# Performance work log

Measured on AMD Instinct MI355X. Metric: run time of the kernel, lower is better.

The kernel has to match this reference:

```python
import jax, jax.numpy as jnp
import numpy as np

B, L, H, C, A = 8, 4096, 512, 64, 512
NEG = -1000000000.0

def setup_inputs() -> dict:
    key = jax.random.key(0)
    ks = jax.random.split(key, 6)
    hidden_states = jax.random.normal(ks[0], (B, L, H), dtype=jnp.float32)
    critical_mask = jax.random.randint(ks[1], (B, L, 1), 0, 2).astype(bool)
    count_active_channels = jax.random.randint(ks[2], (B, L, 1), 0, 64).astype(jnp.int32)
    channel_activity = jax.random.normal(ks[3], (B, L, C), dtype=jnp.float32)
    proj_w = jax.random.normal(ks[4], (H, A), dtype=jnp.float32) * 0.02
    proj_b = jnp.zeros((A,), dtype=jnp.float32)
    score_w = jax.random.normal(ks[5], (A, 1), dtype=jnp.float32) * 0.02
    score_b = jnp.zeros((1,), dtype=jnp.float32)
    return {"hidden_states": hidden_states, "critical_mask": critical_mask,
            "count_active_channels": count_active_channels,
            "channel_activity": channel_activity,
            "proj_w": proj_w, "proj_b": proj_b,
            "score_w": score_w, "score_b": score_b}

def reference(hidden_states, critical_mask, count_active_channels, channel_activity,
              proj_w, proj_b, score_w, score_b):
    mask = critical_mask[..., 0].astype(bool)                       # (B,L)
    count_signal = count_active_channels[..., 0].astype(hidden_states.dtype)  # (B,L)
    activity = jnp.maximum(channel_activity.astype(hidden_states.dtype), 0.0)  # (B,L,C)
    # score(tanh(proj(h)))  -> (B,L)
    logits = (jnp.tanh(hidden_states @ proj_w + proj_b) @ score_w + score_b)[..., 0]
    logits = logits + jnp.log1p(jnp.maximum(count_signal, 0.0))
    channel_mask = activity > 0                                      # (B,L,C)
    # (B,C,L) masked logits with log1p activity bias
    channel_logits = logits[:, None, :] + jnp.log1p(jnp.swapaxes(activity, 1, 2))
    channel_logits = jnp.where(jnp.swapaxes(channel_mask, 1, 2), channel_logits, NEG)
    has_channel_any = channel_mask.any(axis=1)                       # (B,C)
    weights = jax.nn.softmax(channel_logits, axis=-1)                # (B,C,L)
    weights = jnp.where(has_channel_any[..., None], weights, 0.0)
    channel_contexts = jnp.einsum('bcl,blh->bch', weights, hidden_states)  # (B,C,H)
    fallback = jnp.broadcast_to(hidden_states[:, -1:, :], channel_contexts.shape)
    channel_contexts = jnp.where(has_channel_any[..., None], channel_contexts, fallback)
    mix = activity / jnp.maximum(activity.sum(axis=2, keepdims=True), 1.0)  # (B,L,C)
    expanded_context = jnp.einsum('blc,bch->blh', mix, channel_contexts)    # (B,L,H)
    max_count = jnp.maximum(count_signal.max(axis=1, keepdims=True), 1.0)
    density_gate = 1.0 + count_signal / max_count                    # (B,L)
    attended = jnp.where(mask[..., None], expanded_context * density_gate[..., None], hidden_states)
    return attended, weights
```

## Files before the change

kernel.cpp:

```cpp
#include <hip/hip_runtime.h>
#include <hip/hip_bf16.h>
#include <math.h>

#define NEGV (-1000000000.0f)
constexpr int Bb = 8, Ll = 4096, Hh = 512, Cc = 64, Aa = 512;

typedef float f32x4 __attribute__((ext_vector_type(4)));
typedef short s16x8 __attribute__((ext_vector_type(8)));

__device__ inline ushort f2bf(float f) {
  union { float f; uint u; } v; v.f = f;
  uint u = v.u;
  return (ushort)((u + 0x7FFFu + ((u >> 16) & 1u)) >> 16);
}

__device__ inline uint bfpack2(float x, float y) {
  __hip_bfloat162 h = __float22bfloat162_rn(make_float2(x, y));
  union { __hip_bfloat162 h; uint u; } v; v.h = h;
  return v.u;
}

__device__ __forceinline__ void gl16(const void* g, void* l) {
  __builtin_amdgcn_global_load_lds(
      reinterpret_cast<const __attribute__((address_space(1))) unsigned int*>(
          reinterpret_cast<uintptr_t>(g)),
      reinterpret_cast<__attribute__((address_space(3))) unsigned int*>(
          reinterpret_cast<uintptr_t>(l)),
      16, 0, 0);
}

__global__ void k_cvtT(const float* __restrict__ hid, ushort* __restrict__ hidb,
                       ushort* __restrict__ hidbT) {
  __shared__ ushort s[64][65];
  const int b = blockIdx.z;
  const int l0 = blockIdx.x * 64;
  const int h0 = blockIdx.y * 64;
  const int tid = threadIdx.x;
  const int lr = tid >> 6;
  const int hc = tid & 63;
#pragma unroll
  for (int i = 0; i < 16; ++i) {
    int l = lr + i * 4;
    ushort v = f2bf(hid[((size_t)(b * Ll + l0 + l)) * Hh + h0 + hc]);
    s[l][hc] = v;
    hidb[((size_t)(b * Ll + l0 + l)) * Hh + h0 + hc] = v;
  }
  __syncthreads();
#pragma unroll
  for (int i = 0; i < 8; ++i) {
    int e = tid + i * 256;
    int ht = e >> 5, p = e & 31;
    uint v = (uint)s[2 * p][ht] | ((uint)s[2 * p + 1][ht] << 16);
    *(uint*)(hidbT + ((size_t)(b * Hh + h0 + ht)) * Ll + l0 + 2 * p) = v;
  }
}

__global__ void k_init(const int* __restrict__ cnt, const float* __restrict__ sb,
                       float* __restrict__ logits, int* __restrict__ cmax) {
  int i = blockIdx.x * 256 + threadIdx.x;
  int c = cnt[i];
  logits[i] = sb[0] + log1pf(fmaxf((float)c, 0.f));
  int m = c;
#pragma unroll
  for (int s = 32; s; s >>= 1) m = max(m, __shfl_xor(m, s));
  if ((threadIdx.x & 63) == 0) atomicMax(&cmax[i >> 12], m);
}

__global__ void kT_pw(const float* __restrict__ pw, ushort* __restrict__ pwT) {
  __shared__ ushort s[64][65];
  const int k0 = (blockIdx.x >> 3) * 64, a0 = (blockIdx.x & 7) * 64;
  const int t = threadIdx.x;
#pragma unroll
  for (int i = 0; i < 16; ++i) {
    int e = t + i * 256;
    int kk = e >> 6, aa = e & 63;
    s[aa][kk] = f2bf(pw[(size_t)(k0 + kk) * Aa + a0 + aa]);
  }
  __syncthreads();
#pragma unroll
  for (int i = 0; i < 16; ++i) {
    int e = t + i * 256;
    int aa = e >> 6, kk = e & 63;
    pwT[(size_t)(a0 + aa) * Hh + k0 + kk] = s[aa][kk];
  }
}

__global__ __launch_bounds__(256) void k0_gemm(
    const ushort* __restrict__ hidb, const ushort* __restrict__ pwT,
    const float* __restrict__ pb, const float* __restrict__ sw,
    float* __restrict__ logits) {
  __shared__ ushort smem[16384];
  const int bm = blockIdx.x, bn = blockIdx.y;
  const int tid = threadIdx.x;
  const int lane = tid & 63;
  const int w = tid >> 6;
  const int wm = w >> 1, wn = w & 1;
  const int lc = lane & 15, lq = lane >> 4;

  const int srow = tid >> 2;
  const int schunk = (tid & 3) * 8;
  const ushort* Ag = hidb + ((size_t)(bm * 128 + srow)) * Hh + schunk;
  const ushort* Bg = pwT + ((size_t)(bn * 128 + srow)) * Hh + schunk;
  const int wrow = 16 * w;

  f32x4 acc[4][4];
#pragma unroll
  for (int mi = 0; mi < 4; ++mi)
#pragma unroll
    for (int ni = 0; ni < 4; ++ni) acc[mi][ni] = (f32x4){0.f, 0.f, 0.f, 0.f};

  const int aoffc = (wm * 64 + lc) * 32 + lq * 8;
  const int boffc = (wn * 64 + lc) * 32 + lq * 8;

#define K0_STAGE(buf, kb)                                   \
  do {                                                      \
    const ushort* ag = Ag + (kb) * 32;                      \
    const ushort* bg = Bg + (kb) * 32;                      \
    ushort* la = smem + (buf) * 4096 + wrow * 32;           \
    ushort* lb = smem + 8192 + (buf) * 4096 + wrow * 32;    \
    gl16(ag, la);                                           \
    gl16(ag + 64 * Hh, la + 64 * 32);                       \
    gl16(bg, lb);                                           \
    gl16(bg + 64 * Hh, lb + 64 * 32);                       \
  } while (0)

  K0_STAGE(0, 0);
  __syncthreads();

  int buf = 0;
  for (int kb = 0; kb < 16; ++kb) {
    if (kb < 15) K0_STAGE(buf ^ 1, kb + 1);
    const ushort* Ab = smem + buf * 4096;
    const ushort* Bt = smem + 8192 + buf * 4096;
    s16x8 af[4], bfr[4];
#pragma unroll
    for (int mi = 0; mi < 4; ++mi)
      af[mi] = *(const s16x8*)(Ab + aoffc + mi * 512);
#pragma unroll
    for (int ni = 0; ni < 4; ++ni)
      bfr[ni] = *(const s16x8*)(Bt + boffc + ni * 512);
#pragma unroll
    for (int mi = 0; mi < 4; ++mi)
#pragma unroll
      for (int ni = 0; ni < 4; ++ni)
        acc[mi][ni] = __builtin_amdgcn_mfma_f32_16x16x32_bf16(
            af[mi], bfr[ni], acc[mi][ni], 0, 0, 0);
    __syncthreads();
    buf ^= 1;
  }
#undef K0_STAGE

  float pbv[4], swv[4];
#pragma unroll
  for (int ni = 0; ni < 4; ++ni) {
    int n = bn * 128 + wn * 64 + ni * 16 + lc;
    pbv[ni] = pb[n];
    swv[ni] = sw[n];
  }
#pragma unroll
  for (int mi = 0; mi < 4; ++mi) {
#pragma unroll
    for (int r = 0; r < 4; ++r) {
      float s = 0.f;
#pragma unroll
      for (int ni = 0; ni < 4; ++ni) {
        float x = acc[mi][ni][r] + pbv[ni];
        float e = __expf(2.f * x);
        float th = 1.f - 2.f / (e + 1.f);
        s = fmaf(th, swv[ni], s);
      }
      s += __shfl_xor(s, 1);
      s += __shfl_xor(s, 2);
      s += __shfl_xor(s, 4);
      s += __shfl_xor(s, 8);
      if (lc == 0) {
        int m = bm * 128 + wm * 64 + mi * 16 + lq * 4 + r;
        atomicAdd(&logits[m], s);
      }
    }
  }
}

__global__ void k2_transpose(const float* __restrict__ act,
                             float* __restrict__ actT,
                             float* __restrict__ dinv) {
  __shared__ float t64[64][65];
  const int b = blockIdx.x >> 6;
  const int l0 = (blockIdx.x & 63) * 64;
  const int tid = threadIdx.x;
#pragma unroll
  for (int i = 0; i < 16; ++i) {
    int e = tid + i * 256;
    int l = e >> 6, c = e & 63;
    float v = act[((size_t)(b * Ll + l0 + l)) * Cc + c];
    t64[l][c] = fmaxf(v, 0.f);
  }
  __syncthreads();
  if (tid < 64) {
    float s = 0.f;
#pragma unroll 8
    for (int c = 0; c < 64; ++c) s += t64[tid][c];
    dinv[b * Ll + l0 + tid] = 1.0f / fmaxf(s, 1.0f);
  }
#pragma unroll
  for (int i = 0; i < 16; ++i) {
    int e = tid + i * 256;
    int c = e >> 6, lq = e & 63;
    actT[((size_t)(b * Cc + c)) * Ll + l0 + lq] = t64[lq][c];
  }
}

__global__ void k3_softmax(const float* __restrict__ actT,
                           const float* __restrict__ logits,
                           float* __restrict__ wout,
                           ushort* __restrict__ wb16,
                           int* __restrict__ hasany) {
  __shared__ float rmax[4], rcnt[4], rsum[4];
  const int bid = blockIdx.x;
  const int b = bid >> 6;
  const int tid = threadIdx.x;
  const float* arow = actT + (size_t)bid * Ll;

  float xs[16];
  float lmax = NEGV, fcnt = 0.f;
#pragma unroll
  for (int i = 0; i < 16; ++i) {
    int l = tid + i * 256;
    float a = arow[l];
    float x;
    if (a > 0.f) {
      x = logits[b * Ll + l] + log1pf(a);
      fcnt += 1.f;
    } else {
      x = NEGV;
    }
    xs[i] = x;
    lmax = fmaxf(lmax, x);
  }
#pragma unroll
  for (int m = 32; m >= 1; m >>= 1) {
    lmax = fmaxf(lmax, __shfl_xor(lmax, m));
    fcnt += __shfl_xor(fcnt, m);
  }
  if ((tid & 63) == 0) { rmax[tid >> 6] = lmax; rcnt[tid >> 6] = fcnt; }
  __syncthreads();
  float m4 = fmaxf(fmaxf(rmax[0], rmax[1]), fmaxf(rmax[2], rmax[3]));
  float call = rcnt[0] + rcnt[1] + rcnt[2] + rcnt[3];

  float lsum = 0.f;
#pragma unroll
  for (int i = 0; i < 16; ++i) {
    float e = expf(xs[i] - m4);
    xs[i] = e;
    lsum += e;
  }
#pragma unroll
  for (int m = 32; m >= 1; m >>= 1) lsum += __shfl_xor(lsum, m);
  if ((tid & 63) == 0) rsum[tid >> 6] = lsum;
  __syncthreads();
  float s = rsum[0] + rsum[1] + rsum[2] + rsum[3];
  int any = call > 0.5f;
  float inv = any ? 1.0f / s : 0.f;
#pragma unroll
  for (int i = 0; i < 16; ++i) {
    float wv = xs[i] * inv;
    wout[(size_t)bid * Ll + tid + i * 256] = wv;
    wb16[(size_t)bid * Ll + tid + i * 256] = f2bf(wv);
  }
  if (tid == 0) hasany[bid] = any;
}

__global__ __launch_bounds__(256) void k5_mfma(
    const ushort* __restrict__ wb16, const ushort* __restrict__ hidbT,
    float* __restrict__ pbuf) {
  const int b = blockIdx.x, nt = blockIdx.y, kz = blockIdx.z;
  const int tid = threadIdx.x;
  const int w = tid >> 6, lane = tid & 63;
  const int lc = lane & 15, lq = lane >> 4;
  const int h0 = nt * 128 + w * 32;

  f32x4 acc[4][2];
#pragma unroll
  for (int mi = 0; mi < 4; ++mi)
#pragma unroll
    for (int ni = 0; ni < 2; ++ni) acc[mi][ni] = (f32x4){0.f, 0.f, 0.f, 0.f};

  const ushort* Abase =
      wb16 + (size_t)b * Cc * Ll + (size_t)lc * Ll + kz * 256 + lq * 8;
  const ushort* Bbase =
      hidbT + ((size_t)(b * Hh + h0 + lc)) * Ll + kz * 256 + lq * 8;

#pragma unroll 2
  for (int kb = 0; kb < 8; ++kb) {
    s16x8 af[4];
#pragma unroll
    for (int mi = 0; mi < 4; ++mi)
      af[mi] = *(const s16x8*)(Abase + (size_t)mi * 16 * Ll + kb * 32);
    s16x8 bfv[2];
#pragma unroll
    for (int ni = 0; ni < 2; ++ni)
      bfv[ni] = *(const s16x8*)(Bbase + (size_t)ni * 16 * Ll + kb * 32);
#pragma unroll
    for (int mi = 0; mi < 4; ++mi)
#pragma unroll
      for (int ni = 0; ni < 2; ++ni)
        acc[mi][ni] = __builtin_amdgcn_mfma_f32_16x16x32_bf16(
            af[mi], bfv[ni], acc[mi][ni], 0, 0, 0);
  }

  const size_t obase = ((size_t)(kz * Bb + b)) * Cc * Hh;
#pragma unroll
  for (int mi = 0; mi < 4; ++mi)
#pragma unroll
    for (int ni = 0; ni < 2; ++ni)
#pragma unroll
      for (int r = 0; r < 4; ++r)
        pbuf[obase + (size_t)(mi * 16 + lq * 4 + r) * Hh + h0 + ni * 16 + lc] =
            acc[mi][ni][r];
}

__global__ void k6_reduce(const float* __restrict__ pbuf,
                          const int* __restrict__ hasany,
                          const float* __restrict__ hid,
                          float* __restrict__ cctx) {
  int idx = blockIdx.x * 256 + threadIdx.x;
  float s = 0.f;
#pragma unroll
  for (int z = 0; z < 16; ++z) s += pbuf[(size_t)z * 262144 + idx];
  int bc = idx >> 9, b = idx >> 15, h = idx & 511;
  cctx[idx] = hasany[bc] ? s : hid[((size_t)(b * Ll + Ll - 1)) * Hh + h];
}

__global__ __launch_bounds__(256) void k7_out(
    const float* __restrict__ hid, const float* __restrict__ act,
    const float* __restrict__ dinv, const float* __restrict__ cctx,
    const int* __restrict__ mask, const int* __restrict__ cnt,
    const int* __restrict__ cmax, float* __restrict__ out) {
  __shared__ float cct[64][128];
  __shared__ float mixs[64][64];
  __shared__ float gateb[64];
  __shared__ int maskb[64];
  const int b = blockIdx.x;
  const int l0 = blockIdx.y * 64;
  const int h0 = blockIdx.z * 128;
  const int tid = threadIdx.x;
  const int w = tid >> 6;

  {
    const float* g = cctx + (size_t)(b * Cc + (tid >> 5)) * Hh + h0 + (tid & 31) * 4;
    float* lb = &cct[0][0] + (2 * w) * 128;
#pragma unroll
    for (int i = 0; i < 8; ++i)
      gl16(g + (size_t)(i * 8) * Hh, lb + i * 8 * 128);
  }
#pragma unroll
  for (int i = 0; i < 4; ++i) {
    int e = tid + i * 256;
    int t = e >> 4, c4 = (e & 15) * 4;
    float4 a4 = *(const float4*)(act + ((size_t)(b * Ll + l0 + t)) * Cc + c4);
    float dv = dinv[b * Ll + l0 + t];
    a4.x = fmaxf(a4.x, 0.f) * dv;
    a4.y = fmaxf(a4.y, 0.f) * dv;
    a4.z = fmaxf(a4.z, 0.f) * dv;
    a4.w = fmaxf(a4.w, 0.f) * dv;
    *(float4*)&mixs[t][c4] = a4;
  }
  if (tid < 64) {
    int l = l0 + tid;
    maskb[tid] = mask[b * Ll + l];
    gateb[tid] = 1.0f + (float)cnt[b * Ll + l] / fmaxf((float)cmax[b], 1.0f);
  }
  __syncthreads();

  const int hcol = (tid & 31) * 4;
  const int tok0 = (tid >> 5) * 8;

  f32x4 acc[8];
#pragma unroll
  for (int t = 0; t < 8; ++t) acc[t] = (f32x4){0.f, 0.f, 0.f, 0.f};

#pragma unroll 4
  for (int c0 = 0; c0 < 64; c0 += 4) {
    f32x4 cv0 = *(const f32x4*)&cct[c0 + 0][hcol];
    f32x4 cv1 = *(const f32x4*)&cct[c0 + 1][hcol];
    f32x4 cv2 = *(const f32x4*)&cct[c0 + 2][hcol];
    f32x4 cv3 = *(const f32x4*)&cct[c0 + 3][hcol];
#pragma unroll
    for (int t = 0; t < 8; ++t) {
      f32x4 mv = *(const f32x4*)&mixs[tok0 + t][c0];
      f32x4 a = acc[t];
      a = cv0 * mv.x + a;
      a = cv1 * mv.y + a;
      a = cv2 * mv.z + a;
      a = cv3 * mv.w + a;
      acc[t] = a;
    }
  }

#pragma unroll
  for (int t = 0; t < 8; ++t) {
    int tok = tok0 + t;
    size_t off = ((size_t)(b * Ll + l0 + tok)) * Hh + h0 + hcol;
    f32x4 o;
    if (maskb[tok]) {
      o = acc[t] * gateb[tok];
    } else {
      o = *(const f32x4*)(hid + off);
    }
    *(f32x4*)(out + off) = o;
  }
}

extern "C" void kernel_launch(void* const* d_in, const int* in_sizes, int n_in,
                              void* d_out, int out_size, void* d_ws,
                              size_t ws_size, hipStream_t stream) {
  const float* hid = (const float*)d_in[0];
  const int* mask = (const int*)d_in[1];
  const int* cnt = (const int*)d_in[2];
  const float* act = (const float*)d_in[3];
  const float* pw = (const float*)d_in[4];
  const float* pb = (const float*)d_in[5];
  const float* sw = (const float*)d_in[6];
  const float* sb = (const float*)d_in[7];

  float* out_att = (float*)d_out;
  float* out_w = out_att + (size_t)Bb * Ll * Hh;

  float* ws = (float*)d_ws;
  float* cctx = ws;
  int* cmaxi = (int*)(ws + 262144);
  float* logits = ws + 262152;
  float* actT = ws + 294920;
  float* dinv = ws + 2392072;
  int* hasany = (int*)(ws + 2424840);
  ushort* pwT = (ushort*)(ws + 2425352);
  ushort* wb16 = (ushort*)(ws + 2556424);
  float* pbuf = ws + 3605000;

  ushort* hidb = (ushort*)out_att;
  ushort* hidbT = (ushort*)(out_att + 8388608);

  hipMemsetAsync(cmaxi, 0, 8 * sizeof(int), stream);

  k_cvtT<<<dim3(64, 8, 8), 256, 0, stream>>>(hid, hidb, hidbT);
  k_init<<<128, 256, 0, stream>>>(cnt, sb, logits, cmaxi);
  kT_pw<<<64, 256, 0, stream>>>(pw, pwT);
  k0_gemm<<<dim3(256, 4), 256, 0, stream>>>(hidb, pwT, pb, sw, logits);
  k2_transpose<<<512, 256, 0, stream>>>(act, actT, dinv);
  k3_softmax<<<512, 256, 0, stream>>>(actT, logits, out_w, wb16, hasany);
  k5_mfma<<<dim3(8, 4, 16), 256, 0, stream>>>(wb16, hidbT, pbuf);
  k6_reduce<<<1024, 256, 0, stream>>>(pbuf, hasany, hid, cctx);
  k7_out<<<dim3(8, 64, 4), 256, 0, stream>>>(hid, act, dinv, cctx, mask, cnt,
                                             cmaxi, out_att);
}
```

Measured before the change: 265.0 us.

## Replace activity transpose and row softmax with online split-L softmax stats

```diff
diff --git a/kernel.cpp b/kernel.cpp
--- a/kernel.cpp
+++ b/kernel.cpp
@@ -12,12 +12,6 @@
   union { float f; uint u; } v; v.f = f;
   uint u = v.u;
   return (ushort)((u + 0x7FFFu + ((u >> 16) & 1u)) >> 16);
-}
-
-__device__ inline uint bfpack2(float x, float y) {
-  __hip_bfloat162 h = __float22bfloat162_rn(make_float2(x, y));
-  union { __hip_bfloat162 h; uint u; } v; v.h = h;
-  return v.u;
 }
 
 __device__ __forceinline__ void gl16(const void* g, void* l) {
@@ -31,28 +25,35 @@
 
 __global__ void k_cvtT(const float* __restrict__ hid, ushort* __restrict__ hidb,
                        ushort* __restrict__ hidbT) {
-  __shared__ ushort s[64][65];
+  __shared__ ushort s[64][66];
   const int b = blockIdx.z;
   const int l0 = blockIdx.x * 64;
   const int h0 = blockIdx.y * 64;
   const int tid = threadIdx.x;
-  const int lr = tid >> 6;
-  const int hc = tid & 63;
-#pragma unroll
-  for (int i = 0; i < 16; ++i) {
-    int l = lr + i * 4;
-    ushort v = f2bf(hid[((size_t)(b * Ll + l0 + l)) * Hh + h0 + hc]);
-    s[l][hc] = v;
-    hidb[((size_t)(b * Ll + l0 + l)) * Hh + h0 + hc] = v;
-  }
-  __syncthreads();
+  const int lr = tid >> 5;
+  const int hc2 = (tid & 31) * 2;
 #pragma unroll
   for (int i = 0; i < 8; ++i) {
-    int e = tid + i * 256;
-    int ht = e >> 5, p = e & 31;
-    uint v = (uint)s[2 * p][ht] | ((uint)s[2 * p + 1][ht] << 16);
-    *(uint*)(hidbT + ((size_t)(b * Hh + h0 + ht)) * Ll + l0 + 2 * p) = v;
-  }
+    int l = lr * 8 + i;
+    float2 f = *(const float2*)(hid + ((size_t)(b * Ll + l0 + l)) * Hh + h0 + hc2);
+    ushort v0 = f2bf(f.x), v1 = f2bf(f.y);
+    *(uint*)(hidb + ((size_t)(b * Ll + l0 + l)) * Hh + h0 + hc2) =
+        (uint)v0 | ((uint)v1 << 16);
+    s[l][hc2] = v0;
+    s[l][hc2 + 1] = v1;
+  }
+  __syncthreads();
+  const int ht = tid >> 2;
+  const int d0 = (tid & 3) * 8;
+  uint v[8];
+#pragma unroll
+  for (int k = 0; k < 8; ++k) {
+    int p = d0 + k;
+    v[k] = (uint)s[2 * p][ht] | ((uint)s[2 * p + 1][ht] << 16);
+  }
+  ushort* dst = hidbT + ((size_t)(b * Hh + h0 + ht)) * Ll + l0 + 2 * d0;
+  *(uint4*)dst = (uint4){v[0], v[1], v[2], v[3]};
+  *(uint4*)(dst + 8) = (uint4){v[4], v[5], v[6], v[7]};
 }
 
 __global__ void k_init(const int* __restrict__ cnt, const float* __restrict__ sb,
@@ -181,93 +182,128 @@
   }
 }
 
-__global__ void k2_transpose(const float* __restrict__ act,
-                             float* __restrict__ actT,
-                             float* __restrict__ dinv) {
-  __shared__ float t64[64][65];
-  const int b = blockIdx.x >> 6;
-  const int l0 = (blockIdx.x & 63) * 64;
-  const int tid = threadIdx.x;
-#pragma unroll
-  for (int i = 0; i < 16; ++i) {
-    int e = tid + i * 256;
-    int l = e >> 6, c = e & 63;
-    float v = act[((size_t)(b * Ll + l0 + l)) * Cc + c];
-    t64[l][c] = fmaxf(v, 0.f);
+__global__ __launch_bounds__(256) void k2_stats(
+    const float* __restrict__ act, const float* __restrict__ logits,
+    float* __restrict__ dinv, float* __restrict__ part) {
+  __shared__ float Ms[16][64], Ss[16][64];
+  const int b = blockIdx.x, lt = blockIdx.y;
+  const int tid = threadIdx.x;
+  const int r = tid >> 4, cg = (tid & 15) * 4;
+
+  float m[4] = {NEGV, NEGV, NEGV, NEGV};
+  float s[4] = {0.f, 0.f, 0.f, 0.f};
+
+#pragma unroll
+  for (int i = 0; i < 8; ++i) {
+    int l = lt * 128 + r + 16 * i;
+    float lg = logits[b * Ll + l];
+    float4 a4 = *(const float4*)(act + ((size_t)(b * Ll + l)) * Cc + cg);
+    float av[4] = {a4.x, a4.y, a4.z, a4.w};
+    float rsum = 0.f;
+#pragma unroll
+    for (int j = 0; j < 4; ++j) {
+      float a = fmaxf(av[j], 0.f);
+      rsum += a;
+      if (a > 0.f) {
+        float x = lg + log1pf(a);
+        float mn = fmaxf(m[j], x);
+        s[j] = s[j] * expf(m[j] - mn) + expf(x - mn);
+        m[j] = mn;
+      }
+    }
+    rsum += __shfl_xor(rsum, 1);
+    rsum += __shfl_xor(rsum, 2);
+    rsum += __shfl_xor(rsum, 4);
+    rsum += __shfl_xor(rsum, 8);
+    if ((tid & 15) == 0) dinv[b * Ll + l] = 1.0f / fmaxf(rsum, 1.0f);
+  }
+
+#pragma unroll
+  for (int j = 0; j < 4; ++j) {
+    Ms[r][cg + j] = m[j];
+    Ss[r][cg + j] = s[j];
   }
   __syncthreads();
   if (tid < 64) {
-    float s = 0.f;
+    float gm = NEGV, gs = 0.f;
+#pragma unroll
+    for (int rr = 0; rr < 16; ++rr) {
+      float mm = Ms[rr][tid], ss = Ss[rr][tid];
+      float mn = fmaxf(gm, mm);
+      gs = gs * expf(gm - mn) + ss * expf(mm - mn);
+      gm = mn;
+    }
+    size_t o = (((size_t)(b * Cc + tid)) * 32 + lt) * 2;
+    part[o] = gm;
+    part[o + 1] = gs;
+  }
+}
+
+__global__ void k2_merge(const float* __restrict__ part, float* __restrict__ gm,
+                         float* __restrict__ ginv, int* __restrict__ hasany) {
+  int g = blockIdx.x * 256 + threadIdx.x;
+  const float* p = part + (size_t)g * 64;
+  float m = NEGV, s = 0.f;
 #pragma unroll 8
-    for (int c = 0; c < 64; ++c) s += t64[tid][c];
-    dinv[b * Ll + l0 + tid] = 1.0f / fmaxf(s, 1.0f);
-  }
-#pragma unroll
-  for (int i = 0; i < 16; ++i) {
-    int e = tid + i * 256;
-    int c = e >> 6, lq = e & 63;
-    actT[((size_t)(b * Cc + c)) * Ll + l0 + lq] = t64[lq][c];
-  }
-}
-
-__global__ void k3_softmax(const float* __restrict__ actT,
-                           const float* __restrict__ logits,
-                           float* __restrict__ wout,
-                           ushort* __restrict__ wb16,
-                           int* __restrict__ hasany) {
-  __shared__ float rmax[4], rcnt[4], rsum[4];
-  const int bid = blockIdx.x;
-  const int b = bid >> 6;
-  const int tid = threadIdx.x;
-  const float* arow = actT + (size_t)bid * Ll;
-
-  float xs[16];
-  float lmax = NEGV, fcnt = 0.f;
-#pragma unroll
-  for (int i = 0; i < 16; ++i) {
-    int l = tid + i * 256;
-    float a = arow[l];
-    float x;
-    if (a > 0.f) {
-      x = logits[b * Ll + l] + log1pf(a);
-      fcnt += 1.f;
-    } else {
-      x = NEGV;
-    }
-    xs[i] = x;
-    lmax = fmaxf(lmax, x);
-  }
-#pragma unroll
-  for (int m = 32; m >= 1; m >>= 1) {
-    lmax = fmaxf(lmax, __shfl_xor(lmax, m));
-    fcnt += __shfl_xor(fcnt, m);
-  }
-  if ((tid & 63) == 0) { rmax[tid >> 6] = lmax; rcnt[tid >> 6] = fcnt; }
-  __syncthreads();
-  float m4 = fmaxf(fmaxf(rmax[0], rmax[1]), fmaxf(rmax[2], rmax[3]));
-  float call = rcnt[0] + rcnt[1] + rcnt[2] + rcnt[3];
-
-  float lsum = 0.f;
-#pragma unroll
-  for (int i = 0; i < 16; ++i) {
-    float e = expf(xs[i] - m4);
-    xs[i] = e;
-    lsum += e;
-  }
-#pragma unroll
-  for (int m = 32; m >= 1; m >>= 1) lsum += __shfl_xor(lsum, m);
-  if ((tid & 63) == 0) rsum[tid >> 6] = lsum;
-  __syncthreads();
-  float s = rsum[0] + rsum[1] + rsum[2] + rsum[3];
-  int any = call > 0.5f;
-  float inv = any ? 1.0f / s : 0.f;
-#pragma unroll
-  for (int i = 0; i < 16; ++i) {
-    float wv = xs[i] * inv;
-    wout[(size_t)bid * Ll + tid + i * 256] = wv;
-    wb16[(size_t)bid * Ll + tid + i * 256] = f2bf(wv);
-  }
-  if (tid == 0) hasany[bid] = any;
+  for (int t = 0; t < 32; ++t) {
+    float mm = p[2 * t], ss = p[2 * t + 1];
+    float mn = fmaxf(m, mm);
+    s = s * expf(m - mn) + ss * expf(mm - mn);
+    m = mn;
+  }
+  int any = s > 0.5f;
+  gm[g] = m;
+  ginv[g] = any ? 1.0f / s : 0.f;
+  hasany[g] = any;
+}
+
+__global__ __launch_bounds__(256) void k3_weights(
+    const float* __restrict__ act, const float* __restrict__ logits,
+    const float* __restrict__ gm, const float* __restrict__ ginv,
+    float* __restrict__ wout, ushort* __restrict__ wb16) {
+  __shared__ float wls[128][68];
+  const int b = blockIdx.x, lt = blockIdx.y;
+  const int tid = threadIdx.x;
+  const int r = tid >> 4, cg = (tid & 15) * 4;
+
+  float gm4[4], gi4[4];
+#pragma unroll
+  for (int j = 0; j < 4; ++j) {
+    gm4[j] = gm[b * Cc + cg + j];
+    gi4[j] = ginv[b * Cc + cg + j];
+  }
+
+#pragma unroll
+  for (int i = 0; i < 8; ++i) {
+    int l = lt * 128 + r + 16 * i;
+    float lg = logits[b * Ll + l];
+    float4 a4 = *(const float4*)(act + ((size_t)(b * Ll + l)) * Cc + cg);
+    float av[4] = {a4.x, a4.y, a4.z, a4.w};
+    f32x4 wv;
+#pragma unroll
+    for (int j = 0; j < 4; ++j) {
+      float a = fmaxf(av[j], 0.f);
+      float x = lg + log1pf(a);
+      wv[j] = (a > 0.f) ? expf(x - gm4[j]) * gi4[j] : 0.f;
+    }
+    *(f32x4*)&wls[r + 16 * i][cg] = wv;
+  }
+  __syncthreads();
+
+  const int c = tid >> 2;
+  const int ch = (tid & 3) * 32;
+  float* wo = wout + ((size_t)(b * Cc + c)) * Ll + lt * 128 + ch;
+  ushort* wbo = wb16 + ((size_t)(b * Cc + c)) * Ll + lt * 128 + ch;
+#pragma unroll
+  for (int q = 0; q < 8; ++q) {
+    float4 v = make_float4(wls[ch + 4 * q + 0][c], wls[ch + 4 * q + 1][c],
+                           wls[ch + 4 * q + 2][c], wls[ch + 4 * q + 3][c]);
+    *(float4*)(wo + 4 * q) = v;
+    uint2 u;
+    u.x = (uint)f2bf(v.x) | ((uint)f2bf(v.y) << 16);
+    u.y = (uint)f2bf(v.z) | ((uint)f2bf(v.w) << 16);
+    *(uint2*)(wbo + 4 * q) = u;
+  }
 }
 
 __global__ __launch_bounds__(256) void k5_mfma(
@@ -430,12 +466,14 @@
   float* cctx = ws;
   int* cmaxi = (int*)(ws + 262144);
   float* logits = ws + 262152;
-  float* actT = ws + 294920;
-  float* dinv = ws + 2392072;
-  int* hasany = (int*)(ws + 2424840);
-  ushort* pwT = (ushort*)(ws + 2425352);
-  ushort* wb16 = (ushort*)(ws + 2556424);
-  float* pbuf = ws + 3605000;
+  float* dinv = ws + 294920;
+  int* hasany = (int*)(ws + 327688);
+  float* gmbuf = ws + 328200;
+  float* ginvbuf = ws + 328712;
+  float* part = ws + 329224;
+  ushort* pwT = (ushort*)(ws + 361992);
+  ushort* wb16 = (ushort*)(ws + 493064);
+  float* pbuf = ws + 1541640;
 
   ushort* hidb = (ushort*)out_att;
   ushort* hidbT = (ushort*)(out_att + 8388608);
@@ -446,8 +484,10 @@
   k_init<<<128, 256, 0, stream>>>(cnt, sb, logits, cmaxi);
   kT_pw<<<64, 256, 0, stream>>>(pw, pwT);
   k0_gemm<<<dim3(256, 4), 256, 0, stream>>>(hidb, pwT, pb, sw, logits);
-  k2_transpose<<<512, 256, 0, stream>>>(act, actT, dinv);
-  k3_softmax<<<512, 256, 0, stream>>>(actT, logits, out_w, wb16, hasany);
+  k2_stats<<<dim3(8, 32), 256, 0, stream>>>(act, logits, dinv, part);
+  k2_merge<<<2, 256, 0, stream>>>(part, gmbuf, ginvbuf, hasany);
+  k3_weights<<<dim3(8, 32), 256, 0, stream>>>(act, logits, gmbuf, ginvbuf,
+                                              out_w, wb16);
   k5_mfma<<<dim3(8, 4, 16), 256, 0, stream>>>(wb16, hidbT, pbuf);
   k6_reduce<<<1024, 256, 0, stream>>>(pbuf, hasany, hid, cctx);
   k7_out<<<dim3(8, 64, 4), 256, 0, stream>>>(hid, act, dinv, cctx, mask, cnt,
```

Measured after the change: 291.1 us. +9.8%, slower.
